# Kernel optimization log

Hardware: AMD Instinct MI355X
Metric: run time of the kernel (lower is better)

Reference implementation:

```python
import jax, jax.numpy as jnp
import numpy as np

B, N, C_IN, T, K, C_OUT = 16, 1024, 64, 24, 3, 64


def setup_inputs() -> dict:
    key = jax.random.key(0)
    k1, k2, k3, k4 = jax.random.split(key, 4)
    x = jax.random.normal(k1, (B, N, C_IN, T), dtype=jnp.float32)
    STDG = jax.random.uniform(k2, (B, N, N), dtype=jnp.float32)
    cheb = jax.random.normal(k3, (K, N, N), dtype=jnp.float32)
    theta = jax.random.normal(k4, (K, C_IN, C_OUT), dtype=jnp.float32)
    return {"x": x, "STDG": STDG, "cheb": cheb, "theta": theta}


def reference(x, STDG, cheb, theta):
    # x: [B, N, C_in, T]; STDG: [B, N, N]; cheb: [K, N, N]; theta: [K, C_in, C_out]
    # original per (t, k): ((T_k * STDG).T @ x[..., t]) @ theta_k, summed over k, relu
    masked = cheb[:, None, :, :] * STDG[None]              # [K, B, N, N]
    # transpose of masked acts on node dim m: out_n = sum_m masked[k,b,m,n] * x[b,m,c,t]
    rhs = jnp.einsum('kbmn,bmct->kbnct', masked, x)        # [K, B, N, C_in, T]
    out = jnp.einsum('kbnct,kco->bnot', rhs, theta)        # [B, N, C_out, T]
    return jax.nn.relu(out)
```

## Files before the change

kernel.cpp:

```cpp
#include <hip/hip_runtime.h>
#include <stdint.h>


#define BB   16
#define NN   1024
#define CIN  64
#define TT   24
#define KCH  3
#define COUT 64
#define PP   (KCH*NN)
#define JJ   (COUT*TT)

typedef __attribute__((ext_vector_type(4))) float f32x4;
typedef __attribute__((ext_vector_type(8))) short bf16x8;

typedef __attribute__((address_space(1))) const unsigned int* gas_cuintp;
typedef __attribute__((address_space(3))) unsigned int* las_uintp;

static __device__ __forceinline__ unsigned short f2bf(float f){
  union { float f; unsigned u; } v; v.f = f;
  unsigned r = v.u + 0x7fffu + ((v.u >> 16) & 1u);
  return (unsigned short)(r >> 16);
}

__global__ __launch_bounds__(256) void kprepA(const float* __restrict__ cheb,
                                              const float* __restrict__ stdg,
                                              unsigned short* __restrict__ Ah,
                                              int b0, int nb){
  int nt = blockIdx.x;
  int mt = blockIdx.y;
  __shared__ float ct[3][64][65];
  __shared__ float st[64][65];
  int tid = threadIdx.x;
  int rm = tid >> 2;
  int nc = (tid & 3) << 4;
  #pragma unroll
  for (int k = 0; k < 3; k++){
    const float* cp = cheb + ((size_t)(k*NN + mt*64 + rm))*NN + nt*64 + nc;
    #pragma unroll
    for (int i = 0; i < 16; i += 4){
      f32x4 cv = *(const f32x4*)(cp + i);
      #pragma unroll
      for (int q = 0; q < 4; q++) ct[k][nc + i + q][rm] = cv[q];
    }
  }
  int rn = tid >> 2;
  int mc = (tid & 3) << 4;
  for (int bb = 0; bb < nb; bb++){
    int b = b0 + bb;
    __syncthreads();
    const float* sp = stdg + ((size_t)(b*NN + mt*64 + rm))*NN + nt*64 + nc;
    #pragma unroll
    for (int i = 0; i < 16; i += 4){
      f32x4 sv = *(const f32x4*)(sp + i);
      #pragma unroll
      for (int q = 0; q < 4; q++) st[nc + i + q][rm] = sv[q];
    }
    __syncthreads();
    #pragma unroll
    for (int k = 0; k < 3; k++){
      union { unsigned short s[16]; uint4 v[2]; } hb;
      #pragma unroll
      for (int i = 0; i < 16; i++) hb.s[i] = f2bf(ct[k][rn][mc + i] * st[rn][mc + i]);
      size_t ob = ((size_t)(bb*NN + nt*64 + rn))*PP + (size_t)k*NN + mt*64 + mc;
      *(uint4*)(Ah + ob)     = hb.v[0];
      *(uint4*)(Ah + ob + 8) = hb.v[1];
    }
  }
}

__global__ __launch_bounds__(256) void kprepY(const float* __restrict__ x,
                                              const float* __restrict__ theta,
                                              unsigned short* __restrict__ Yt,
                                              int b0){
  int ms = blockIdx.x;
  int jb = blockIdx.y;
  int bb = blockIdx.z;
  int b  = b0 + bb;
  __shared__ float xs[32*196];
  __shared__ float ths[3*64*8];
  __shared__ unsigned short ytile[192*32];
  int tid = threadIdx.x;
  int mi = tid >> 3, oi = tid & 7;

  for (int i = tid; i < 3*64*8; i += 256){
    int k = i >> 9, rem = i & 511;
    int c = rem >> 3, o = rem & 7;
    ths[i] = theta[k*(CIN*COUT) + c*COUT + jb*8 + o];
  }

  float acc0[24], acc1[24], acc2[24];
  #pragma unroll
  for (int t = 0; t < 24; t++){ acc0[t]=0.f; acc1[t]=0.f; acc2[t]=0.f; }

  const f32x4* xg4 = (const f32x4*)(x + ((size_t)(b*NN + ms*32))*CIN*TT);

  int pm[6], pr[6];
  #pragma unroll
  for (int u = 0; u < 6; u++){
    int i4 = tid + u*256;
    pm[u] = i4 / 48; pr[u] = i4 - pm[u]*48;
  }
  f32x4 pf[6];
  #pragma unroll
  for (int u = 0; u < 6; u++) pf[u] = xg4[pm[u]*384 + pr[u]];

  for (int cc = 0; cc < 8; cc++){
    __syncthreads();
    #pragma unroll
    for (int u = 0; u < 6; u++) *(f32x4*)&xs[pm[u]*196 + pr[u]*4] = pf[u];
    __syncthreads();
    if (cc < 7){
      #pragma unroll
      for (int u = 0; u < 6; u++) pf[u] = xg4[pm[u]*384 + (cc+1)*48 + pr[u]];
    }
    for (int c8 = 0; c8 < 8; c8++){
      float xv[24];
      #pragma unroll
      for (int q = 0; q < 6; q++) *(f32x4*)&xv[q*4] = *(const f32x4*)&xs[mi*196 + c8*24 + q*4];
      int cg = cc*8 + c8;
      float t0 = ths[0*512 + cg*8 + oi];
      float t1 = ths[1*512 + cg*8 + oi];
      float t2 = ths[2*512 + cg*8 + oi];
      #pragma unroll
      for (int t = 0; t < 24; t++){
        acc0[t] = fmaf(t0, xv[t], acc0[t]);
        acc1[t] = fmaf(t1, xv[t], acc1[t]);
        acc2[t] = fmaf(t2, xv[t], acc2[t]);
      }
    }
  }

  #pragma unroll
  for (int k = 0; k < 3; k++){
    const float* a = (k==0) ? acc0 : (k==1) ? acc1 : acc2;
    __syncthreads();
    #pragma unroll
    for (int t = 0; t < 24; t++){
      int row = oi*24 + t;
      int sw  = (row >> 3) & 3;
      int sc  = (mi >> 3) ^ sw;
      ytile[row*32 + sc*8 + (mi & 7)] = f2bf(a[t]);
    }
    __syncthreads();
    for (int r = 0; r < 3; r++){
      int i   = tid + r*256;
      int row = i >> 2, c4 = i & 3;
      int sw  = (row >> 3) & 3;
      uint4 v = *(const uint4*)&ytile[row*32 + (c4 ^ sw)*8];
      size_t ob = ((size_t)bb*JJ + (size_t)jb*192 + row)*PP + k*NN + ms*32 + c4*8;
      *(uint4*)(Yt + ob) = v;
    }
  }
}

__global__ __launch_bounds__(256, 2) void kgemm(
    const unsigned short* __restrict__ Ah,
    const unsigned short* __restrict__ Yh,
    float* __restrict__ out, int b0){
  __shared__ unsigned short AsL[128*64];
  __shared__ unsigned short YsL[128*64];
  int orig = blockIdx.x;
  int cpx  = (int)(gridDim.x >> 3);
  int wgid = ((orig & 7) * cpx) + (orig >> 3);
  int bb  = wgid / 96;
  int r96 = wgid - bb*96;
  int nt  = r96 / 12;
  int jt  = r96 - nt*12;
  int tid = threadIdx.x;
  int lane = tid & 63, wave = tid >> 6;
  int wr = wave >> 1, wc = wave & 1;

  unsigned aoff[4], yoff[4];
  #pragma unroll
  for (int it = 0; it < 4; it++){
    int c = tid + it*256;
    int row = c >> 3;
    int sc = (c & 7) ^ (row & 7);
    aoff[it] = (unsigned)(((bb*NN + nt*128 + row) * PP) * 2 + sc * 16);
    yoff[it] = (unsigned)(((bb*JJ + jt*128 + row) * PP) * 2 + sc * 16);
  }

  f32x4 acc[4][4];
  #pragma unroll
  for (int i = 0; i < 4; i++)
    #pragma unroll
    for (int q = 0; q < 4; q++) acc[i][q] = (f32x4){0.f, 0.f, 0.f, 0.f};

  unsigned ldsw = (unsigned)(wave * 1024);
  const char* pA = (const char*)Ah;
  const char* pY = (const char*)Yh;

  for (int ps = 0; ps < PP/64; ps++){
    unsigned so = (unsigned)(ps * 128);
    #pragma unroll
    for (int it = 0; it < 4; it++){
      unsigned ld = ldsw + it*4096;
      __builtin_amdgcn_global_load_lds((gas_cuintp)(pA + aoff[it] + so), (las_uintp)((char*)AsL + ld), 16, 0, 0);
      __builtin_amdgcn_global_load_lds((gas_cuintp)(pY + yoff[it] + so), (las_uintp)((char*)YsL + ld), 16, 0, 0);
    }
    __syncthreads();
    #pragma unroll
    for (int kk = 0; kk < 2; kk++){
      bf16x8 a_f[4], y_f[4];
      #pragma unroll
      for (int i = 0; i < 4; i++){
        int arow = wr*64 + i*16 + (lane & 15);
        int ach  = ((kk*4) + (lane >> 4)) ^ (arow & 7);
        a_f[i] = *(const bf16x8*)&AsL[arow*64 + ach*8];
        int jrow = wc*64 + i*16 + (lane & 15);
        int jch  = ((kk*4) + (lane >> 4)) ^ (jrow & 7);
        y_f[i] = *(const bf16x8*)&YsL[jrow*64 + jch*8];
      }
      #pragma unroll
      for (int i = 0; i < 4; i++)
        #pragma unroll
        for (int q = 0; q < 4; q++)
          acc[i][q] = __builtin_amdgcn_mfma_f32_16x16x32_bf16(a_f[i], y_f[q], acc[i][q], 0, 0, 0);
    }
    __syncthreads();
  }
  size_t ob = (size_t)(b0 + bb) * NN * JJ;
  #pragma unroll
  for (int i = 0; i < 4; i++){
    int nbase = nt*128 + wr*64 + i*16 + ((lane >> 4) << 2);
    #pragma unroll
    for (int q = 0; q < 4; q++){
      int j = jt*128 + wc*64 + q*16 + (lane & 15);
      #pragma unroll
      for (int e = 0; e < 4; e++){
        float v = acc[i][q][e];
        v = v > 0.f ? v : 0.f;
        out[ob + (size_t)(nbase + e) * JJ + j] = v;
      }
    }
  }
}

extern "C" void kernel_launch(void* const* d_in, const int* in_sizes, int n_in,
                              void* d_out, int out_size, void* d_ws, size_t ws_size,
                              hipStream_t stream){
  (void)in_sizes; (void)n_in; (void)out_size;
  const float* x     = (const float*)d_in[0];
  const float* stdg  = (const float*)d_in[1];
  const float* cheb  = (const float*)d_in[2];
  const float* theta = (const float*)d_in[3];
  float* out = (float*)d_out;

  const size_t szA_b = (size_t)NN * PP * sizeof(unsigned short);
  const size_t szY_b = (size_t)PP * JJ * sizeof(unsigned short);
  const size_t per_b = szA_b + szY_b;
  int NB = 16;
  while (NB > 1 && per_b * (size_t)NB > ws_size) NB >>= 1;

  char* w = (char*)d_ws;
  unsigned short* Ah = (unsigned short*)w;                         w += szA_b * NB;
  unsigned short* Yt = (unsigned short*)w;                         w += szY_b * NB;

  for (int b0 = 0; b0 < BB; b0 += NB){
    kprepA<<<dim3(16, 16),    256, 0, stream>>>(cheb, stdg, Ah, b0, NB);
    kprepY<<<dim3(32, 8, NB), 256, 0, stream>>>(x, theta, Yt, b0);
    kgemm<<<dim3(NB*96),      256, 0, stream>>>(Ah, Yt, out, b0);
  }
}
```

Before: 539.7 us.

## Rewrite GEMM as 256x256 tile, 8-wave, double-buffered LDS pipeline

The GEMM kernel moves to 256x256 output tiles with 512 threads (8 waves, 2x4 layout). Each wave computes a 128x64 sub-tile. LDS is double-buffered, and global-to-LDS loads for the next K step are interleaved with MFMA blocks, using explicit barriers, waitcnts and s_setprio. The goal is to hide global latency and raise data reuse per block. The trade-off is about 128KB of LDS per block, and only 384 blocks to spread over the CUs, which risks wave-quantization tail imbalance.

```diff
diff --git a/kernel.cpp b/kernel.cpp
--- a/kernel.cpp
+++ b/kernel.cpp
@@ -154,84 +154,185 @@
   }
 }
 
-__global__ __launch_bounds__(256, 2) void kgemm(
+#define STG_A(kkv, t1) { \
+    unsigned so = (unsigned)((t1)*128 + (kkv)*64); \
+    unsigned ld = (unsigned)((((t1)&1)*32768) + (kkv)*16384) + wbase; \
+    __builtin_amdgcn_global_load_lds((gas_cuintp)(pA + aoff0 + so), (las_uintp)(ldsA + ld), 16, 0, 0); \
+    __builtin_amdgcn_global_load_lds((gas_cuintp)(pA + aoff1 + so), (las_uintp)(ldsA + ld + 8192), 16, 0, 0); }
+#define STG_Y(kkv, t1) { \
+    unsigned so = (unsigned)((t1)*128 + (kkv)*64); \
+    unsigned ld = (unsigned)((((t1)&1)*32768) + (kkv)*16384) + wbase; \
+    __builtin_amdgcn_global_load_lds((gas_cuintp)(pY + yoff0 + so), (las_uintp)(ldsY + ld), 16, 0, 0); \
+    __builtin_amdgcn_global_load_lds((gas_cuintp)(pY + yoff1 + so), (las_uintp)(ldsY + ld + 8192), 16, 0, 0); }
+#define FENCE_BAR  { __builtin_amdgcn_sched_barrier(0); __builtin_amdgcn_s_barrier(); }
+#define LGKM_WAIT  { asm volatile("s_waitcnt lgkmcnt(0)" ::: "memory"); __builtin_amdgcn_sched_barrier(0); }
+
+__global__ __launch_bounds__(512, 2) void kgemm(
     const unsigned short* __restrict__ Ah,
     const unsigned short* __restrict__ Yh,
     float* __restrict__ out, int b0){
-  __shared__ unsigned short AsL[128*64];
-  __shared__ unsigned short YsL[128*64];
+  __shared__ unsigned short AsL[32768];
+  __shared__ unsigned short YsL[32768];
   int orig = blockIdx.x;
   int cpx  = (int)(gridDim.x >> 3);
   int wgid = ((orig & 7) * cpx) + (orig >> 3);
-  int bb  = wgid / 96;
-  int r96 = wgid - bb*96;
-  int nt  = r96 / 12;
-  int jt  = r96 - nt*12;
+  int bb  = wgid / 24;
+  int r24 = wgid - bb*24;
+  int nt  = r24 / 6;
+  int jt  = r24 - nt*6;
   int tid = threadIdx.x;
   int lane = tid & 63, wave = tid >> 6;
-  int wr = wave >> 1, wc = wave & 1;
-
-  unsigned aoff[4], yoff[4];
-  #pragma unroll
-  for (int it = 0; it < 4; it++){
-    int c = tid + it*256;
-    int row = c >> 3;
-    int sc = (c & 7) ^ (row & 7);
-    aoff[it] = (unsigned)(((bb*NN + nt*128 + row) * PP) * 2 + sc * 16);
-    yoff[it] = (unsigned)(((bb*JJ + jt*128 + row) * PP) * 2 + sc * 16);
-  }
-
-  f32x4 acc[4][4];
-  #pragma unroll
-  for (int i = 0; i < 4; i++)
-    #pragma unroll
-    for (int q = 0; q < 4; q++) acc[i][q] = (f32x4){0.f, 0.f, 0.f, 0.f};
-
-  unsigned ldsw = (unsigned)(wave * 1024);
+  int wr = wave >> 2, wc = wave & 3;
+
+  int r0 = tid >> 2, c0 = tid & 3;
+  unsigned aoff0 = (unsigned)((bb*NN + nt*256 + r0) * (PP*2)) + (unsigned)(c0*16);
+  unsigned aoff1 = aoff0 + (unsigned)(128 * PP * 2);
+  unsigned yoff0 = (unsigned)((bb*JJ + jt*256 + r0) * (PP*2)) + (unsigned)(c0*16);
+  unsigned yoff1 = yoff0 + (unsigned)(128 * PP * 2);
   const char* pA = (const char*)Ah;
   const char* pY = (const char*)Yh;
-
-  for (int ps = 0; ps < PP/64; ps++){
-    unsigned so = (unsigned)(ps * 128);
-    #pragma unroll
-    for (int it = 0; it < 4; it++){
-      unsigned ld = ldsw + it*4096;
-      __builtin_amdgcn_global_load_lds((gas_cuintp)(pA + aoff[it] + so), (las_uintp)((char*)AsL + ld), 16, 0, 0);
-      __builtin_amdgcn_global_load_lds((gas_cuintp)(pY + yoff[it] + so), (las_uintp)((char*)YsL + ld), 16, 0, 0);
-    }
-    __syncthreads();
-    #pragma unroll
-    for (int kk = 0; kk < 2; kk++){
-      bf16x8 a_f[4], y_f[4];
-      #pragma unroll
-      for (int i = 0; i < 4; i++){
-        int arow = wr*64 + i*16 + (lane & 15);
-        int ach  = ((kk*4) + (lane >> 4)) ^ (arow & 7);
-        a_f[i] = *(const bf16x8*)&AsL[arow*64 + ach*8];
-        int jrow = wc*64 + i*16 + (lane & 15);
-        int jch  = ((kk*4) + (lane >> 4)) ^ (jrow & 7);
-        y_f[i] = *(const bf16x8*)&YsL[jrow*64 + jch*8];
-      }
-      #pragma unroll
-      for (int i = 0; i < 4; i++)
-        #pragma unroll
-        for (int q = 0; q < 4; q++)
-          acc[i][q] = __builtin_amdgcn_mfma_f32_16x16x32_bf16(a_f[i], y_f[q], acc[i][q], 0, 0, 0);
-    }
-    __syncthreads();
-  }
+  char* ldsA = (char*)AsL;
+  char* ldsY = (char*)YsL;
+  unsigned wbase = (unsigned)(wave * 1024);
+
+  int athr = (wr*128 + (lane & 15))*32 + (lane >> 4)*8;
+  int ythr = (wc*64  + (lane & 15))*32 + (lane >> 4)*8;
+
+  f32x4 acc[8][4];
+  #pragma unroll
+  for (int m = 0; m < 8; m++)
+    #pragma unroll
+    for (int q = 0; q < 4; q++) acc[m][q] = (f32x4){0.f, 0.f, 0.f, 0.f};
+
+  bf16x8 af[4], yf[4];
+
+  STG_A(0, 0); STG_Y(0, 0); STG_A(1, 0); STG_Y(1, 0);
+  asm volatile("s_waitcnt vmcnt(4)" ::: "memory");
+  __builtin_amdgcn_s_barrier();
+
+  for (int t = 0; t < PP/64 - 1; t++){
+    int cur = (t & 1) * 16384;
+    #pragma unroll
+    for (int i = 0; i < 4; i++){
+      af[i] = *(const bf16x8*)&AsL[cur + i*512 + athr];
+      yf[i] = *(const bf16x8*)&YsL[cur + i*512 + ythr];
+    }
+    STG_A(0, t+1);
+    FENCE_BAR; LGKM_WAIT;
+    __builtin_amdgcn_s_setprio(1);
+    #pragma unroll
+    for (int m = 0; m < 4; m++)
+      #pragma unroll
+      for (int q = 0; q < 4; q++)
+        acc[m][q] = __builtin_amdgcn_mfma_f32_16x16x32_bf16(af[m], yf[q], acc[m][q], 0, 0, 0);
+    __builtin_amdgcn_s_setprio(0);
+    FENCE_BAR;
+    #pragma unroll
+    for (int i = 0; i < 4; i++)
+      af[i] = *(const bf16x8*)&AsL[cur + 2048 + i*512 + athr];
+    STG_Y(0, t+1);
+    FENCE_BAR; LGKM_WAIT;
+    __builtin_amdgcn_s_setprio(1);
+    #pragma unroll
+    for (int m = 0; m < 4; m++)
+      #pragma unroll
+      for (int q = 0; q < 4; q++)
+        acc[4+m][q] = __builtin_amdgcn_mfma_f32_16x16x32_bf16(af[m], yf[q], acc[4+m][q], 0, 0, 0);
+    __builtin_amdgcn_s_setprio(0);
+    asm volatile("s_waitcnt vmcnt(4)" ::: "memory");
+    FENCE_BAR;
+    #pragma unroll
+    for (int i = 0; i < 4; i++){
+      af[i] = *(const bf16x8*)&AsL[cur + 8192 + i*512 + athr];
+      yf[i] = *(const bf16x8*)&YsL[cur + 8192 + i*512 + ythr];
+    }
+    STG_A(1, t+1);
+    FENCE_BAR; LGKM_WAIT;
+    __builtin_amdgcn_s_setprio(1);
+    #pragma unroll
+    for (int m = 0; m < 4; m++)
+      #pragma unroll
+      for (int q = 0; q < 4; q++)
+        acc[m][q] = __builtin_amdgcn_mfma_f32_16x16x32_bf16(af[m], yf[q], acc[m][q], 0, 0, 0);
+    __builtin_amdgcn_s_setprio(0);
+    FENCE_BAR;
+    #pragma unroll
+    for (int i = 0; i < 4; i++)
+      af[i] = *(const bf16x8*)&AsL[cur + 8192 + 2048 + i*512 + athr];
+    STG_Y(1, t+1);
+    FENCE_BAR; LGKM_WAIT;
+    __builtin_amdgcn_s_setprio(1);
+    #pragma unroll
+    for (int m = 0; m < 4; m++)
+      #pragma unroll
+      for (int q = 0; q < 4; q++)
+        acc[4+m][q] = __builtin_amdgcn_mfma_f32_16x16x32_bf16(af[m], yf[q], acc[4+m][q], 0, 0, 0);
+    __builtin_amdgcn_s_setprio(0);
+    asm volatile("s_waitcnt vmcnt(4)" ::: "memory");
+    FENCE_BAR;
+  }
+
+  {
+    int cur = ((PP/64 - 1) & 1) * 16384;
+    #pragma unroll
+    for (int i = 0; i < 4; i++){
+      af[i] = *(const bf16x8*)&AsL[cur + i*512 + athr];
+      yf[i] = *(const bf16x8*)&YsL[cur + i*512 + ythr];
+    }
+    FENCE_BAR; LGKM_WAIT;
+    #pragma unroll
+    for (int m = 0; m < 4; m++)
+      #pragma unroll
+      for (int q = 0; q < 4; q++)
+        acc[m][q] = __builtin_amdgcn_mfma_f32_16x16x32_bf16(af[m], yf[q], acc[m][q], 0, 0, 0);
+    FENCE_BAR;
+    #pragma unroll
+    for (int i = 0; i < 4; i++)
+      af[i] = *(const bf16x8*)&AsL[cur + 2048 + i*512 + athr];
+    FENCE_BAR; LGKM_WAIT;
+    #pragma unroll
+    for (int m = 0; m < 4; m++)
+      #pragma unroll
+      for (int q = 0; q < 4; q++)
+        acc[4+m][q] = __builtin_amdgcn_mfma_f32_16x16x32_bf16(af[m], yf[q], acc[4+m][q], 0, 0, 0);
+    asm volatile("s_waitcnt vmcnt(0)" ::: "memory");
+    FENCE_BAR;
+    #pragma unroll
+    for (int i = 0; i < 4; i++){
+      af[i] = *(const bf16x8*)&AsL[cur + 8192 + i*512 + athr];
+      yf[i] = *(const bf16x8*)&YsL[cur + 8192 + i*512 + ythr];
+    }
+    FENCE_BAR; LGKM_WAIT;
+    #pragma unroll
+    for (int m = 0; m < 4; m++)
+      #pragma unroll
+      for (int q = 0; q < 4; q++)
+        acc[m][q] = __builtin_amdgcn_mfma_f32_16x16x32_bf16(af[m], yf[q], acc[m][q], 0, 0, 0);
+    FENCE_BAR;
+    #pragma unroll
+    for (int i = 0; i < 4; i++)
+      af[i] = *(const bf16x8*)&AsL[cur + 8192 + 2048 + i*512 + athr];
+    LGKM_WAIT;
+    #pragma unroll
+    for (int m = 0; m < 4; m++)
+      #pragma unroll
+      for (int q = 0; q < 4; q++)
+        acc[4+m][q] = __builtin_amdgcn_mfma_f32_16x16x32_bf16(af[m], yf[q], acc[4+m][q], 0, 0, 0);
+  }
+
   size_t ob = (size_t)(b0 + bb) * NN * JJ;
-  #pragma unroll
-  for (int i = 0; i < 4; i++){
-    int nbase = nt*128 + wr*64 + i*16 + ((lane >> 4) << 2);
+  int jbase = jt*256 + wc*64 + (lane & 15);
+  int nbase = nt*256 + wr*128 + ((lane >> 4) << 2);
+  #pragma unroll
+  for (int m = 0; m < 8; m++){
     #pragma unroll
     for (int q = 0; q < 4; q++){
-      int j = jt*128 + wc*64 + q*16 + (lane & 15);
+      int j = jbase + q*16;
       #pragma unroll
       for (int e = 0; e < 4; e++){
-        float v = acc[i][q][e];
+        float v = acc[m][q][e];
         v = v > 0.f ? v : 0.f;
-        out[ob + (size_t)(nbase + e) * JJ + j] = v;
+        out[ob + (size_t)(nbase + m*16 + e) * JJ + j] = v;
       }
     }
   }
@@ -260,6 +361,6 @@
   for (int b0 = 0; b0 < BB; b0 += NB){
     kprepA<<<dim3(16, 16),    256, 0, stream>>>(cheb, stdg, Ah, b0, NB);
     kprepY<<<dim3(32, 8, NB), 256, 0, stream>>>(x, theta, Yt, b0);
-    kgemm<<<dim3(NB*96),      256, 0, stream>>>(Ah, Yt, out, b0);
-  }
-}
+    kgemm<<<dim3(NB*24),      512, 0, stream>>>(Ah, Yt, out, b0);
+  }
+}
```

Result: slower. 616.7 us (+14.3%).
